# Kernel optimization log

Hardware: AMD Instinct MI355X
Metric: run time of the kernel (lower is better)

## Reference

```python
import jax, jax.numpy as jnp
from jax import lax
import numpy as np

B, H, W_, C, F = 4, 32, 32, 16, 16
KH, KW = 3, 3
L = 1.0


def setup_inputs() -> dict:
    key = jax.random.key(0)
    k1, k2, k3, k4 = jax.random.split(key, 4)
    inputs = jax.random.normal(k1, (B, H, W_, C), dtype=jnp.float32)
    # lecun_normal-style scales (stddev = 1/sqrt(fan_in))
    m_scale = 1.0 / np.sqrt(H * W_ * 1)
    g_scale = 1.0 / np.sqrt(KH * KW * C)
    M = jax.random.normal(k2, (H, W_, 1, H, W_, 1), dtype=jnp.float32) * m_scale
    Wp = jax.random.normal(k3, (H, W_, 1, H, W_, 1), dtype=jnp.float32) * m_scale
    G = jax.random.normal(k4, (H, W_, KH, KW, C, F), dtype=jnp.float32) * g_scale
    return {"inputs": inputs, "M": M, "Wp": Wp, "G": G}


def reference(inputs, M, Wp, G):
    b, h, w, c = inputs.shape
    kh, kw, f = G.shape[2], G.shape[3], G.shape[5]
    M2 = M[:, :, 0, :, :, 0]   # (i,j,p,q)
    W2 = Wp[:, :, 0, :, :, 0]  # (i,j,p,q)
    # first_term[b,i,j,c] = sum_pq M[i,j,p,q] * inputs[b,p,q,c]
    first = jnp.einsum('ijpq,bpqc->bijc', M2, inputs)
    # One big conv: kernel (kh,kw,c, h*w*f) gives shifted for every output pixel (i,j)
    K = jnp.transpose(G, (2, 3, 4, 0, 1, 5)).reshape(kh, kw, c, h * w * f)
    shifted = lax.conv_general_dilated(
        inputs, K, window_strides=(1, 1), padding='SAME',
        dimension_numbers=('NHWC', 'HWIO', 'NHWC'))
    shifted = shifted.reshape(b, h, w, h, w, f)  # (b,p,q,i,j,f)
    diff = jax.nn.relu(inputs[:, :, :, None, None, :] - shifted)  # (b,p,q,i,j,c)
    # second_term[b,i,j,c] = sum_pq W[i,j,p,q] * relu(inputs - shifted)[b,p,q,i,j,c]
    second = jnp.einsum('ijpq,bpqijc->bijc', W2, diff)
    return first - L * second
```

## Files before the change

kernel.cpp:

```cpp
#include <hip/hip_runtime.h>


typedef __attribute__((ext_vector_type(8))) short bf16x8;
typedef __attribute__((ext_vector_type(4))) float f32x4;

__device__ inline unsigned short f2bf(float x) {
    unsigned u = __float_as_uint(x);
    u += 0x7FFFu + ((u >> 16) & 1u);
    return (unsigned short)(u >> 16);
}
__device__ inline unsigned pack2(float a, float b) {
    return (unsigned)f2bf(a) | ((unsigned)f2bf(b) << 16);
}

__device__ inline void gld_lds16(const void* g, void* l) {
    __builtin_amdgcn_global_load_lds((const __attribute__((address_space(1))) void*)g,
                                     (__attribute__((address_space(3))) void*)l, 16, 0, 0);
}

__global__ __launch_bounds__(256) void build_pre(const float* __restrict__ inp,
                                                 const float* __restrict__ G,
                                                 uint4* __restrict__ A,
                                                 float4* __restrict__ Xf,
                                                 uint4* __restrict__ Gf,
                                                 float4* __restrict__ outz) {
    const int tid = blockIdx.x * 256 + threadIdx.x;
    const int u = tid >> 12;
    if (u >= 28) {
        const int gidx = tid - 114688;
        const int ijkk = gidx >> 6, l = gidx & 63;
        const int ij = ijkk / 5, kk = ijkk - ij * 5;
        const int quad = l >> 4, col = l & 15;
        const float* Gg = G + ij * 2304;
        float v[8];
#pragma unroll
        for (int j = 0; j < 8; ++j) {
            const int k = kk * 32 + quad * 8 + j;
            v[j] = (k < 144) ? Gg[k * 16 + col] : 0.f;
        }
        uint4 o;
        o.x = pack2(v[0], v[1]); o.y = pack2(v[2], v[3]);
        o.z = pack2(v[4], v[5]); o.w = pack2(v[6], v[7]);
        Gf[ij * 320 + kk * 64 + l] = o;
        return;
    }
    if (u >= 24) {
        outz[tid - 98304] = (float4){0.f, 0.f, 0.f, 0.f};
        return;
    }
    if (u >= 20) {
        const int idx = tid - 81920;
        const int tile = idx >> 6, ll = idx & 63;
        const int rowb = tile * 16 + (ll >> 4) * 4;
        const int col = ll & 15;
        float4 v;
        v.x = inp[(rowb + 0) * 16 + col];
        v.y = inp[(rowb + 1) * 16 + col];
        v.z = inp[(rowb + 2) * 16 + col];
        v.w = inp[(rowb + 3) * 16 + col];
        Xf[idx] = v;
        return;
    }
    const int row = tid & 4095;
    const int tile = row >> 4, m = row & 15;
    if (u >= 18) {
        const uint4 z = {0, 0, 0, 0};
        A[(tile * 5 + 4) * 64 + (u - 16) * 16 + m] = z;
        return;
    }
    const int tap = u >> 1, h = u & 1;
    const int dh = tap / 3, dw = tap - dh * 3;
    const int b = row >> 10, pq = row & 1023;
    const int p = pq >> 5, q = pq & 31;
    const int pp = p + dh - 1, qq = q + dw - 1;
    const int kk = tap >> 1, quad = (tap & 1) * 2 + h;
    uint4 o = {0, 0, 0, 0};
    if (((unsigned)pp < 32u) && ((unsigned)qq < 32u)) {
        const float4* s = (const float4*)(inp + b * 16384 + (pp * 32 + qq) * 16 + 8 * h);
        const float4 f0 = s[0], f1 = s[1];
        o.x = pack2(f0.x, f0.y); o.y = pack2(f0.z, f0.w);
        o.z = pack2(f1.x, f1.y); o.w = pack2(f1.z, f1.w);
    }
    A[(tile * 5 + kk) * 64 + quad * 16 + m] = o;
}

__global__ __launch_bounds__(512, 2) void inrf_main(
    const float* __restrict__ M,
    const float* __restrict__ Wp,
    const uint4* __restrict__ Gf,
    const uint4* __restrict__ Aw,
    const float4* __restrict__ Xf,
    float* __restrict__ out)
{
    const int bid = blockIdx.x;
    const int ijblk = bid & 31;
    const int tgrp  = bid >> 5;
    const int tile0 = tgrp * 16;
    const int bb    = tgrp >> 2;

    const int t = threadIdx.x, l = t & 63, w = t >> 6;
    const int quad = l >> 4;

    __shared__ __align__(16) uint4  Ab[2][4][5][64];
    __shared__ __align__(16) float4 Xb[2][4][64];

    auto stage = [&](int buf, int ct0) {
#pragma unroll
        for (int r = 0; r < 3; ++r) {
            const int s = w * 3 + r;
            if (s < 20) {
                const int ct = s / 5, kk = s - ct * 5;
                gld_lds16(&Aw[((ct0 + ct) * 5 + kk) * 64 + l], &Ab[buf][ct][kk][0]);
            } else {
                const int ct = s - 20;
                gld_lds16(&Xf[(ct0 + ct) * 64 + l], &Xb[buf][ct][0]);
            }
        }
    };

    stage(0, tile0);

    const int ij0 = ijblk * 32 + w * 4;
    bf16x8 Bf[4][5];
#pragma unroll
    for (int ij = 0; ij < 4; ++ij)
#pragma unroll
        for (int kk = 0; kk < 5; ++kk)
            Bf[ij][kk] = __builtin_bit_cast(bf16x8, Gf[(ij0 + ij) * 320 + kk * 64 + l]);

    float accv[4] = {0.f, 0.f, 0.f, 0.f};

    asm volatile("s_waitcnt vmcnt(0)" ::: "memory");
    __syncthreads();

    int buf = 0;
#pragma unroll 1
    for (int ph = 0; ph < 4; ++ph) {
        if (ph < 3) stage(buf ^ 1, tile0 + (ph + 1) * 4);
#pragma unroll
        for (int ct = 0; ct < 4; ++ct) {
            const int tg = tile0 + ph * 4 + ct;
            uint4 Af[5];
#pragma unroll
            for (int kk = 0; kk < 5; ++kk) Af[kk] = Ab[buf][ct][kk][l];
            const float4 vr = Xb[buf][ct][l];

            f32x4 C[4];
#pragma unroll
            for (int jj = 0; jj < 4; ++jj) C[jj] = (f32x4){0.f, 0.f, 0.f, 0.f};
#pragma unroll
            for (int kk = 0; kk < 5; ++kk) {
                const bf16x8 a = __builtin_bit_cast(bf16x8, Af[kk]);
#pragma unroll
                for (int jj = 0; jj < 4; ++jj)
                    C[jj] = __builtin_amdgcn_mfma_f32_16x16x32_bf16(
                                a, Bf[jj][kk], C[jj], 0, 0, 0);
            }

            const int pqb = (tg & 63) * 16 + quad * 4;
#pragma unroll
            for (int jj = 0; jj < 4; ++jj) {
                const int ijg = ij0 + jj;
                const float4 w2 = *(const float4*)&Wp[ijg * 1024 + pqb];
                const float4 m2 = *(const float4*)&M [ijg * 1024 + pqb];
                float a0 = accv[jj];
                a0 += m2.x * vr.x - w2.x * fmaxf(vr.x - C[jj][0], 0.f);
                a0 += m2.y * vr.y - w2.y * fmaxf(vr.y - C[jj][1], 0.f);
                a0 += m2.z * vr.z - w2.z * fmaxf(vr.z - C[jj][2], 0.f);
                a0 += m2.w * vr.w - w2.w * fmaxf(vr.w - C[jj][3], 0.f);
                accv[jj] = a0;
            }
        }
        asm volatile("s_waitcnt vmcnt(0)" ::: "memory");
        __syncthreads();
        buf ^= 1;
    }

#pragma unroll
    for (int jj = 0; jj < 4; ++jj) {
        float v = accv[jj];
        v += __shfl_xor(v, 16);
        v += __shfl_xor(v, 32);
        if (l < 16) atomicAdd(&out[bb * 16384 + (ij0 + jj) * 16 + l], v);
    }
}

extern "C" void kernel_launch(void* const* d_in, const int* in_sizes, int n_in,
                              void* d_out, int out_size, void* d_ws, size_t ws_size,
                              hipStream_t stream) {
    const float* inp = (const float*)d_in[0];
    const float* M   = (const float*)d_in[1];
    const float* Wp  = (const float*)d_in[2];
    const float* G   = (const float*)d_in[3];
    float* out = (float*)d_out;

    uint4*  A  = (uint4*)d_ws;
    float4* Xf = (float4*)((char*)d_ws + 1310720);
    uint4*  Gf = (uint4*)((char*)d_ws + 1572864);

    build_pre<<<dim3(1728), dim3(256), 0, stream>>>(inp, G, A, Xf, Gf, (float4*)out);
    inrf_main<<<dim3(512), dim3(512), 0, stream>>>(M, Wp, Gf, A, Xf, out);
}
```

Baseline: 101.8 us.

## Switch to 32x32 MFMA tiles with block-owned output pixels and LDS-cached M/W

Restructures the main kernel so each block owns four output pixels (ij) across all batch tiles, using 32x32x16 bf16 MFMAs with 32-row tiles and the K dimension split per tap. M and Wp slices are staged once into LDS, and the A/X operands are read straight from global memory instead of through the double-buffered LDS staging. Results are reduced across waves in shared memory and written directly, which removes the atomics and the output-zeroing pass. The grid shrinks to 256 blocks at occupancy 1, which lowers parallelism and latency hiding in exchange for more reuse per block.

```diff
diff --git a/kernel.cpp b/kernel.cpp
--- a/kernel.cpp
+++ b/kernel.cpp
@@ -2,7 +2,7 @@
 
 
 typedef __attribute__((ext_vector_type(8))) short bf16x8;
-typedef __attribute__((ext_vector_type(4))) float f32x4;
+typedef __attribute__((ext_vector_type(16))) float f32x16;
 
 __device__ inline unsigned short f2bf(float x) {
     unsigned u = __float_as_uint(x);
@@ -13,78 +13,66 @@
     return (unsigned)f2bf(a) | ((unsigned)f2bf(b) << 16);
 }
 
-__device__ inline void gld_lds16(const void* g, void* l) {
-    __builtin_amdgcn_global_load_lds((const __attribute__((address_space(1))) void*)g,
-                                     (__attribute__((address_space(3))) void*)l, 16, 0, 0);
-}
-
 __global__ __launch_bounds__(256) void build_pre(const float* __restrict__ inp,
                                                  const float* __restrict__ G,
                                                  uint4* __restrict__ A,
                                                  float4* __restrict__ Xf,
-                                                 uint4* __restrict__ Gf,
-                                                 float4* __restrict__ outz) {
+                                                 uint4* __restrict__ Gf) {
     const int tid = blockIdx.x * 256 + threadIdx.x;
     const int u = tid >> 12;
-    if (u >= 28) {
-        const int gidx = tid - 114688;
-        const int ijkk = gidx >> 6, l = gidx & 63;
-        const int ij = ijkk / 5, kk = ijkk - ij * 5;
-        const int quad = l >> 4, col = l & 15;
-        const float* Gg = G + ij * 2304;
-        float v[8];
-#pragma unroll
-        for (int j = 0; j < 8; ++j) {
-            const int k = kk * 32 + quad * 8 + j;
-            v[j] = (k < 144) ? Gg[k * 16 + col] : 0.f;
+    if (u >= 24) {
+        const int gidx = tid - 98304;
+        const int lane = gidx & 63;
+        const int rem = gidx >> 6;
+        const int ij2 = rem / 10, s = rem - ij2 * 10;
+        const int col = lane & 31, h = lane >> 5;
+        const int ij = ij2 * 2 + (col >> 4), f = col & 15;
+        uint4 o = {0, 0, 0, 0};
+        if (s < 9) {
+            const float* Gg = G + ij * 2304 + s * 256 + h * 128 + f;
+            o.x = pack2(Gg[0],  Gg[16]);
+            o.y = pack2(Gg[32], Gg[48]);
+            o.z = pack2(Gg[64], Gg[80]);
+            o.w = pack2(Gg[96], Gg[112]);
         }
-        uint4 o;
-        o.x = pack2(v[0], v[1]); o.y = pack2(v[2], v[3]);
-        o.z = pack2(v[4], v[5]); o.w = pack2(v[6], v[7]);
-        Gf[ij * 320 + kk * 64 + l] = o;
-        return;
-    }
-    if (u >= 24) {
-        outz[tid - 98304] = (float4){0.f, 0.f, 0.f, 0.f};
+        Gf[gidx] = o;
         return;
     }
     if (u >= 20) {
         const int idx = tid - 81920;
-        const int tile = idx >> 6, ll = idx & 63;
-        const int rowb = tile * 16 + (ll >> 4) * 4;
-        const int col = ll & 15;
+        const int f = idx & 15, g = (idx >> 4) & 3, lh = (idx >> 6) & 1, T = idx >> 7;
+        const int rb = T * 32 + g * 8 + lh * 4;
         float4 v;
-        v.x = inp[(rowb + 0) * 16 + col];
-        v.y = inp[(rowb + 1) * 16 + col];
-        v.z = inp[(rowb + 2) * 16 + col];
-        v.w = inp[(rowb + 3) * 16 + col];
+        v.x = inp[(rb + 0) * 16 + f];
+        v.y = inp[(rb + 1) * 16 + f];
+        v.z = inp[(rb + 2) * 16 + f];
+        v.w = inp[(rb + 3) * 16 + f];
         Xf[idx] = v;
         return;
     }
-    const int row = tid & 4095;
-    const int tile = row >> 4, m = row & 15;
     if (u >= 18) {
-        const uint4 z = {0, 0, 0, 0};
-        A[(tile * 5 + 4) * 64 + (u - 16) * 16 + m] = z;
+        const int flat = (u - 18) * 4096 + (tid & 4095);
+        A[((flat >> 6) * 10 + 9) * 64 + (flat & 63)] = (uint4){0, 0, 0, 0};
         return;
     }
+    const int row = tid & 4095;
     const int tap = u >> 1, h = u & 1;
+    const int T = row >> 5;
     const int dh = tap / 3, dw = tap - dh * 3;
     const int b = row >> 10, pq = row & 1023;
     const int p = pq >> 5, q = pq & 31;
     const int pp = p + dh - 1, qq = q + dw - 1;
-    const int kk = tap >> 1, quad = (tap & 1) * 2 + h;
     uint4 o = {0, 0, 0, 0};
     if (((unsigned)pp < 32u) && ((unsigned)qq < 32u)) {
-        const float4* s = (const float4*)(inp + b * 16384 + (pp * 32 + qq) * 16 + 8 * h);
-        const float4 f0 = s[0], f1 = s[1];
+        const float4* s4 = (const float4*)(inp + b * 16384 + (pp * 32 + qq) * 16 + 8 * h);
+        const float4 f0 = s4[0], f1 = s4[1];
         o.x = pack2(f0.x, f0.y); o.y = pack2(f0.z, f0.w);
         o.z = pack2(f1.x, f1.y); o.w = pack2(f1.z, f1.w);
     }
-    A[(tile * 5 + kk) * 64 + quad * 16 + m] = o;
+    A[(T * 10 + tap) * 64 + h * 32 + (row & 31)] = o;
 }
 
-__global__ __launch_bounds__(512, 2) void inrf_main(
+__global__ __launch_bounds__(512, 1) void inrf_main(
     const float* __restrict__ M,
     const float* __restrict__ Wp,
     const uint4* __restrict__ Gf,
@@ -93,95 +81,87 @@
     float* __restrict__ out)
 {
     const int bid = blockIdx.x;
-    const int ijblk = bid & 31;
-    const int tgrp  = bid >> 5;
-    const int tile0 = tgrp * 16;
-    const int bb    = tgrp >> 2;
+    const int t = threadIdx.x, l = t & 63, w = t >> 6;
 
-    const int t = threadIdx.x, l = t & 63, w = t >> 6;
-    const int quad = l >> 4;
+    __shared__ __align__(16) float W2l[4096];
+    __shared__ __align__(16) float M2l[4096];
+    __shared__ float red[8][64];
 
-    __shared__ __align__(16) uint4  Ab[2][4][5][64];
-    __shared__ __align__(16) float4 Xb[2][4][64];
+    {
+        const float4* Wg = (const float4*)(Wp + bid * 4096);
+        const float4* Mg = (const float4*)(M  + bid * 4096);
+        float4* W4 = (float4*)W2l;
+        float4* M4 = (float4*)M2l;
+        W4[t] = Wg[t]; W4[t + 512] = Wg[t + 512];
+        M4[t] = Mg[t]; M4[t + 512] = Mg[t + 512];
+    }
 
-    auto stage = [&](int buf, int ct0) {
+    bf16x8 Bf[2][10];
 #pragma unroll
-        for (int r = 0; r < 3; ++r) {
-            const int s = w * 3 + r;
-            if (s < 20) {
-                const int ct = s / 5, kk = s - ct * 5;
-                gld_lds16(&Aw[((ct0 + ct) * 5 + kk) * 64 + l], &Ab[buf][ct][kk][0]);
-            } else {
-                const int ct = s - 20;
-                gld_lds16(&Xf[(ct0 + ct) * 64 + l], &Xb[buf][ct][0]);
+    for (int p = 0; p < 2; ++p)
+#pragma unroll
+        for (int s = 0; s < 10; ++s)
+            Bf[p][s] = __builtin_bit_cast(bf16x8, Gf[((bid * 2 + p) * 10 + s) * 64 + l]);
+
+    __syncthreads();
+
+    const int lh = l >> 5;
+    const int ijb = (l >> 4) & 1;
+    const int xcol = l & 15;
+    float acc0 = 0.f, acc1 = 0.f;
+
+    const int T0 = w * 16;
+#pragma unroll 2
+    for (int i = 0; i < 16; ++i) {
+        const int T = T0 + i;
+
+        uint4 Af[10];
+#pragma unroll
+        for (int s = 0; s < 10; ++s) Af[s] = Aw[(T * 10 + s) * 64 + l];
+        float4 xv[4];
+#pragma unroll
+        for (int g = 0; g < 4; ++g) xv[g] = Xf[(T * 2 + lh) * 64 + g * 16 + xcol];
+
+        f32x16 C0 = {0.f}, C1 = {0.f};
+#pragma unroll
+        for (int s = 0; s < 10; ++s) {
+            const bf16x8 a = __builtin_bit_cast(bf16x8, Af[s]);
+            C0 = __builtin_amdgcn_mfma_f32_32x32x16_bf16(a, Bf[0][s], C0, 0, 0, 0);
+            C1 = __builtin_amdgcn_mfma_f32_32x32x16_bf16(a, Bf[1][s], C1, 0, 0, 0);
+        }
+
+        const int pqb = (T & 31) * 32 + lh * 4;
+#pragma unroll
+        for (int g = 0; g < 4; ++g) {
+            const float4 xg = xv[g];
+            {
+                const float4 w2 = *(const float4*)&W2l[ijb * 1024 + pqb + g * 8];
+                const float4 m2 = *(const float4*)&M2l[ijb * 1024 + pqb + g * 8];
+                acc0 += m2.x * xg.x - w2.x * fmaxf(xg.x - C0[g * 4 + 0], 0.f);
+                acc0 += m2.y * xg.y - w2.y * fmaxf(xg.y - C0[g * 4 + 1], 0.f);
+                acc0 += m2.z * xg.z - w2.z * fmaxf(xg.z - C0[g * 4 + 2], 0.f);
+                acc0 += m2.w * xg.w - w2.w * fmaxf(xg.w - C0[g * 4 + 3], 0.f);
+            }
+            {
+                const float4 w2 = *(const float4*)&W2l[(2 + ijb) * 1024 + pqb + g * 8];
+                const float4 m2 = *(const float4*)&M2l[(2 + ijb) * 1024 + pqb + g * 8];
+                acc1 += m2.x * xg.x - w2.x * fmaxf(xg.x - C1[g * 4 + 0], 0.f);
+                acc1 += m2.y * xg.y - w2.y * fmaxf(xg.y - C1[g * 4 + 1], 0.f);
+                acc1 += m2.z * xg.z - w2.z * fmaxf(xg.z - C1[g * 4 + 2], 0.f);
+                acc1 += m2.w * xg.w - w2.w * fmaxf(xg.w - C1[g * 4 + 3], 0.f);
             }
         }
-    };
+    }
 
-    stage(0, tile0);
-
-    const int ij0 = ijblk * 32 + w * 4;
-    bf16x8 Bf[4][5];
-#pragma unroll
-    for (int ij = 0; ij < 4; ++ij)
-#pragma unroll
-        for (int kk = 0; kk < 5; ++kk)
-            Bf[ij][kk] = __builtin_bit_cast(bf16x8, Gf[(ij0 + ij) * 320 + kk * 64 + l]);
-
-    float accv[4] = {0.f, 0.f, 0.f, 0.f};
-
-    asm volatile("s_waitcnt vmcnt(0)" ::: "memory");
+    acc0 += __shfl_xor(acc0, 32);
+    acc1 += __shfl_xor(acc1, 32);
+    if (l < 32) { red[w][l] = acc0; red[w][32 + l] = acc1; }
     __syncthreads();
 
-    int buf = 0;
-#pragma unroll 1
-    for (int ph = 0; ph < 4; ++ph) {
-        if (ph < 3) stage(buf ^ 1, tile0 + (ph + 1) * 4);
-#pragma unroll
-        for (int ct = 0; ct < 4; ++ct) {
-            const int tg = tile0 + ph * 4 + ct;
-            uint4 Af[5];
-#pragma unroll
-            for (int kk = 0; kk < 5; ++kk) Af[kk] = Ab[buf][ct][kk][l];
-            const float4 vr = Xb[buf][ct][l];
-
-            f32x4 C[4];
-#pragma unroll
-            for (int jj = 0; jj < 4; ++jj) C[jj] = (f32x4){0.f, 0.f, 0.f, 0.f};
-#pragma unroll
-            for (int kk = 0; kk < 5; ++kk) {
-                const bf16x8 a = __builtin_bit_cast(bf16x8, Af[kk]);
-#pragma unroll
-                for (int jj = 0; jj < 4; ++jj)
-                    C[jj] = __builtin_amdgcn_mfma_f32_16x16x32_bf16(
-                                a, Bf[jj][kk], C[jj], 0, 0, 0);
-            }
-
-            const int pqb = (tg & 63) * 16 + quad * 4;
-#pragma unroll
-            for (int jj = 0; jj < 4; ++jj) {
-                const int ijg = ij0 + jj;
-                const float4 w2 = *(const float4*)&Wp[ijg * 1024 + pqb];
-                const float4 m2 = *(const float4*)&M [ijg * 1024 + pqb];
-                float a0 = accv[jj];
-                a0 += m2.x * vr.x - w2.x * fmaxf(vr.x - C[jj][0], 0.f);
-                a0 += m2.y * vr.y - w2.y * fmaxf(vr.y - C[jj][1], 0.f);
-                a0 += m2.z * vr.z - w2.z * fmaxf(vr.z - C[jj][2], 0.f);
-                a0 += m2.w * vr.w - w2.w * fmaxf(vr.w - C[jj][3], 0.f);
-                accv[jj] = a0;
-            }
-        }
-        asm volatile("s_waitcnt vmcnt(0)" ::: "memory");
-        __syncthreads();
-        buf ^= 1;
-    }
-
-#pragma unroll
-    for (int jj = 0; jj < 4; ++jj) {
-        float v = accv[jj];
-        v += __shfl_xor(v, 16);
-        v += __shfl_xor(v, 32);
-        if (l < 16) atomicAdd(&out[bb * 16384 + (ij0 + jj) * 16 + l], v);
+    if (t < 256) {
+        const int ob = t >> 6, oij = (t >> 4) & 3, oc = t & 15;
+        const int idx = (oij >> 1) * 32 + (oij & 1) * 16 + oc;
+        out[ob * 16384 + (bid * 4 + oij) * 16 + oc] = red[ob * 2][idx] + red[ob * 2 + 1][idx];
     }
 }
 
@@ -198,6 +178,6 @@
     float4* Xf = (float4*)((char*)d_ws + 1310720);
     uint4*  Gf = (uint4*)((char*)d_ws + 1572864);
 
-    build_pre<<<dim3(1728), dim3(256), 0, stream>>>(inp, G, A, Xf, Gf, (float4*)out);
-    inrf_main<<<dim3(512), dim3(512), 0, stream>>>(M, Wp, Gf, A, Xf, out);
+    build_pre<<<dim3(1664), dim3(256), 0, stream>>>(inp, G, A, Xf, Gf);
+    inrf_main<<<dim3(256), dim3(512), 0, stream>>>(M, Wp, Gf, A, Xf, out);
 }
```

After: 125.1 us. 1.23x slower.

## Split first term into prep kernel and repartition main kernel per ij block

Applied to the files above, without the earlier changes.

Moves the M·inputs first term into a separate reduction section of the prep kernel, which writes it to a workspace buffer. The main kernel now gives each block four ij outputs across all batches and tiles, and stages that block's Wp rows in LDS. A/X tiles are register double-buffered from global memory instead of async-copied into LDS. Results are reduced within the block and written directly, with no atomics or output zeroing. The price is half as many blocks, a serial 1024-term dot product per thread in the prep kernel, and heavier register use.

```diff
diff --git a/kernel.cpp b/kernel.cpp
--- a/kernel.cpp
+++ b/kernel.cpp
@@ -13,21 +13,28 @@
     return (unsigned)f2bf(a) | ((unsigned)f2bf(b) << 16);
 }
 
-__device__ inline void gld_lds16(const void* g, void* l) {
-    __builtin_amdgcn_global_load_lds((const __attribute__((address_space(1))) void*)g,
-                                     (__attribute__((address_space(3))) void*)l, 16, 0, 0);
-}
-
 __global__ __launch_bounds__(256) void build_pre(const float* __restrict__ inp,
+                                                 const float* __restrict__ Mm,
                                                  const float* __restrict__ G,
                                                  uint4* __restrict__ A,
                                                  float4* __restrict__ Xf,
                                                  uint4* __restrict__ Gf,
-                                                 float4* __restrict__ outz) {
+                                                 float* __restrict__ F) {
     const int tid = blockIdx.x * 256 + threadIdx.x;
     const int u = tid >> 12;
-    if (u >= 28) {
-        const int gidx = tid - 114688;
+    if (u >= 104) {
+        const int idx = tid - 425984;
+        const int ij = idx >> 6, b = (idx >> 4) & 3, c = idx & 15;
+        const float* Mg = Mm + ij * 1024;
+        const float* xb = inp + b * 16384 + c;
+        float s = 0.f;
+#pragma unroll 8
+        for (int pq = 0; pq < 1024; ++pq) s = __builtin_fmaf(Mg[pq], xb[pq * 16], s);
+        F[b * 16384 + ij * 16 + c] = s;
+        return;
+    }
+    if (u >= 24) {
+        const int gidx = tid - 98304;
         const int ijkk = gidx >> 6, l = gidx & 63;
         const int ij = ijkk / 5, kk = ijkk - ij * 5;
         const int quad = l >> 4, col = l & 15;
@@ -42,10 +49,6 @@
         o.x = pack2(v[0], v[1]); o.y = pack2(v[2], v[3]);
         o.z = pack2(v[4], v[5]); o.w = pack2(v[6], v[7]);
         Gf[ij * 320 + kk * 64 + l] = o;
-        return;
-    }
-    if (u >= 24) {
-        outz[tid - 98304] = (float4){0.f, 0.f, 0.f, 0.f};
         return;
     }
     if (u >= 20) {
@@ -76,8 +79,8 @@
     const int kk = tap >> 1, quad = (tap & 1) * 2 + h;
     uint4 o = {0, 0, 0, 0};
     if (((unsigned)pp < 32u) && ((unsigned)qq < 32u)) {
-        const float4* s = (const float4*)(inp + b * 16384 + (pp * 32 + qq) * 16 + 8 * h);
-        const float4 f0 = s[0], f1 = s[1];
+        const float4* s4 = (const float4*)(inp + b * 16384 + (pp * 32 + qq) * 16 + 8 * h);
+        const float4 f0 = s4[0], f1 = s4[1];
         o.x = pack2(f0.x, f0.y); o.y = pack2(f0.z, f0.w);
         o.z = pack2(f1.x, f1.y); o.w = pack2(f1.z, f1.w);
     }
@@ -85,103 +88,99 @@
 }
 
 __global__ __launch_bounds__(512, 2) void inrf_main(
-    const float* __restrict__ M,
     const float* __restrict__ Wp,
     const uint4* __restrict__ Gf,
     const uint4* __restrict__ Aw,
-    const float4* __restrict__ Xf,
+    const f32x4* __restrict__ Xf,
+    const float* __restrict__ F,
     float* __restrict__ out)
 {
     const int bid = blockIdx.x;
-    const int ijblk = bid & 31;
-    const int tgrp  = bid >> 5;
-    const int tile0 = tgrp * 16;
-    const int bb    = tgrp >> 2;
-
     const int t = threadIdx.x, l = t & 63, w = t >> 6;
     const int quad = l >> 4;
 
-    __shared__ __align__(16) uint4  Ab[2][4][5][64];
-    __shared__ __align__(16) float4 Xb[2][4][64];
-
-    auto stage = [&](int buf, int ct0) {
-#pragma unroll
-        for (int r = 0; r < 3; ++r) {
-            const int s = w * 3 + r;
-            if (s < 20) {
-                const int ct = s / 5, kk = s - ct * 5;
-                gld_lds16(&Aw[((ct0 + ct) * 5 + kk) * 64 + l], &Ab[buf][ct][kk][0]);
-            } else {
-                const int ct = s - 20;
-                gld_lds16(&Xf[(ct0 + ct) * 64 + l], &Xb[buf][ct][0]);
-            }
+    __shared__ __align__(16) float W2l[4096];
+    __shared__ float red[8][64];
+
+    {
+        const float4* Wg = (const float4*)(Wp + bid * 4096);
+        float4* W4 = (float4*)W2l;
+        W4[t] = Wg[t]; W4[t + 512] = Wg[t + 512];
+    }
+
+    const int ij0 = bid * 4;
+    bf16x8 Bf[4][5];
+#pragma unroll
+    for (int ij = 0; ij < 4; ++ij)
+#pragma unroll
+        for (int kk = 0; kk < 5; ++kk)
+            Bf[ij][kk] = __builtin_bit_cast(bf16x8, Gf[(ij0 + ij) * 320 + kk * 64 + l]);
+
+    __syncthreads();
+
+    const int b = w >> 1;
+    const int tile0 = b * 64 + (w & 1) * 32;
+
+    f32x4 accv[4];
+#pragma unroll
+    for (int jj = 0; jj < 4; ++jj) accv[jj] = (f32x4){0.f, 0.f, 0.f, 0.f};
+
+    uint4 A0[5], A1[5];
+    f32x4 v0, v1;
+
+    auto prefetch = [&](uint4 (&Ar)[5], f32x4& vr, int tn) {
+#pragma unroll
+        for (int kk = 0; kk < 5; ++kk) Ar[kk] = Aw[(tn * 5 + kk) * 64 + l];
+        vr = Xf[tn * 64 + l];
+    };
+
+    const f32x4 zero4 = (f32x4){0.f, 0.f, 0.f, 0.f};
+
+    auto compute = [&](const uint4 (&Ar)[5], const f32x4& vr, int tg) {
+        f32x4 C[4];
+#pragma unroll
+        for (int jj = 0; jj < 4; ++jj) C[jj] = zero4;
+#pragma unroll
+        for (int kk = 0; kk < 5; ++kk) {
+            const bf16x8 a = __builtin_bit_cast(bf16x8, Ar[kk]);
+#pragma unroll
+            for (int jj = 0; jj < 4; ++jj)
+                C[jj] = __builtin_amdgcn_mfma_f32_16x16x32_bf16(a, Bf[jj][kk], C[jj], 0, 0, 0);
+        }
+        const int pqb = (tg & 63) * 16 + quad * 4;
+#pragma unroll
+        for (int jj = 0; jj < 4; ++jj) {
+            const f32x4 w2 = *(const f32x4*)&W2l[jj * 1024 + pqb];
+            const f32x4 d = vr - C[jj];
+            const f32x4 r = __builtin_elementwise_max(d, zero4);
+            accv[jj] += w2 * r;
         }
     };
 
-    stage(0, tile0);
-
-    const int ij0 = ijblk * 32 + w * 4;
-    bf16x8 Bf[4][5];
-#pragma unroll
-    for (int ij = 0; ij < 4; ++ij)
-#pragma unroll
-        for (int kk = 0; kk < 5; ++kk)
-            Bf[ij][kk] = __builtin_bit_cast(bf16x8, Gf[(ij0 + ij) * 320 + kk * 64 + l]);
-
-    float accv[4] = {0.f, 0.f, 0.f, 0.f};
-
-    asm volatile("s_waitcnt vmcnt(0)" ::: "memory");
-    __syncthreads();
-
-    int buf = 0;
+    prefetch(A0, v0, tile0);
 #pragma unroll 1
-    for (int ph = 0; ph < 4; ++ph) {
-        if (ph < 3) stage(buf ^ 1, tile0 + (ph + 1) * 4);
-#pragma unroll
-        for (int ct = 0; ct < 4; ++ct) {
-            const int tg = tile0 + ph * 4 + ct;
-            uint4 Af[5];
-#pragma unroll
-            for (int kk = 0; kk < 5; ++kk) Af[kk] = Ab[buf][ct][kk][l];
-            const float4 vr = Xb[buf][ct][l];
-
-            f32x4 C[4];
-#pragma unroll
-            for (int jj = 0; jj < 4; ++jj) C[jj] = (f32x4){0.f, 0.f, 0.f, 0.f};
-#pragma unroll
-            for (int kk = 0; kk < 5; ++kk) {
-                const bf16x8 a = __builtin_bit_cast(bf16x8, Af[kk]);
-#pragma unroll
-                for (int jj = 0; jj < 4; ++jj)
-                    C[jj] = __builtin_amdgcn_mfma_f32_16x16x32_bf16(
-                                a, Bf[jj][kk], C[jj], 0, 0, 0);
-            }
-
-            const int pqb = (tg & 63) * 16 + quad * 4;
-#pragma unroll
-            for (int jj = 0; jj < 4; ++jj) {
-                const int ijg = ij0 + jj;
-                const float4 w2 = *(const float4*)&Wp[ijg * 1024 + pqb];
-                const float4 m2 = *(const float4*)&M [ijg * 1024 + pqb];
-                float a0 = accv[jj];
-                a0 += m2.x * vr.x - w2.x * fmaxf(vr.x - C[jj][0], 0.f);
-                a0 += m2.y * vr.y - w2.y * fmaxf(vr.y - C[jj][1], 0.f);
-                a0 += m2.z * vr.z - w2.z * fmaxf(vr.z - C[jj][2], 0.f);
-                a0 += m2.w * vr.w - w2.w * fmaxf(vr.w - C[jj][3], 0.f);
-                accv[jj] = a0;
-            }
-        }
-        asm volatile("s_waitcnt vmcnt(0)" ::: "memory");
-        __syncthreads();
-        buf ^= 1;
+    for (int i = 0; i < 32; i += 2) {
+        prefetch(A1, v1, tile0 + i + 1);
+        compute(A0, v0, tile0 + i);
+        if (i + 2 < 32) prefetch(A0, v0, tile0 + i + 2);
+        compute(A1, v1, tile0 + i + 1);
     }
 
 #pragma unroll
     for (int jj = 0; jj < 4; ++jj) {
-        float v = accv[jj];
+        const f32x4 a = accv[jj];
+        float v = (a[0] + a[1]) + (a[2] + a[3]);
         v += __shfl_xor(v, 16);
         v += __shfl_xor(v, 32);
-        if (l < 16) atomicAdd(&out[bb * 16384 + (ij0 + jj) * 16 + l], v);
+        if (l < 16) red[w][jj * 16 + l] = v;
+    }
+    __syncthreads();
+
+    if (t < 256) {
+        const int ob = t >> 6, oij = (t >> 4) & 3, oc = t & 15;
+        const float r0 = red[ob * 2][oij * 16 + oc] + red[ob * 2 + 1][oij * 16 + oc];
+        const int o = ob * 16384 + (ij0 + oij) * 16 + oc;
+        out[o] = F[o] - r0;
     }
 }
 
@@ -197,7 +196,8 @@
     uint4*  A  = (uint4*)d_ws;
     float4* Xf = (float4*)((char*)d_ws + 1310720);
     uint4*  Gf = (uint4*)((char*)d_ws + 1572864);
-
-    build_pre<<<dim3(1728), dim3(256), 0, stream>>>(inp, G, A, Xf, Gf, (float4*)out);
-    inrf_main<<<dim3(512), dim3(512), 0, stream>>>(M, Wp, Gf, A, Xf, out);
-}
+    float*  F  = (float*)((char*)d_ws + 6815744);
+
+    build_pre<<<dim3(1920), dim3(256), 0, stream>>>(inp, M, G, A, Xf, Gf, F);
+    inrf_main<<<dim3(256), dim3(512), 0, stream>>>(Wp, Gf, A, (const f32x4*)Xf, F, out);
+}
```

After: 127.6 us. 25.3% more time.
